# Kernel tuning notes

Measured on AMD Instinct MI355X. Metric: run time of the kernel, lower is better.

## Reference

```python
import jax, jax.numpy as jnp
import numpy as np

N_EMBED = 8192
EMBED_DIM = 256
DECAY = 0.99
EPS = 1e-05


def setup_inputs() -> dict:
    key = jax.random.key(0)
    k1, k2 = jax.random.split(key)
    z = jax.random.normal(k1, (16, 32, 32, EMBED_DIM), dtype=jnp.float32)
    weight = jax.random.normal(k2, (N_EMBED, EMBED_DIM), dtype=jnp.float32)
    cluster_size = jnp.zeros((N_EMBED,), dtype=jnp.float32)
    embed_avg = weight  # register_buffer initialized as a clone of the embedding weight
    return {"z": z, "weight": weight, "cluster_size": cluster_size, "embed_avg": embed_avg}


def reference(z, weight, cluster_size, embed_avg):
    # use_norm=False -> norm is identity; training=True branch; straight_through=True
    zf = z.reshape(-1, EMBED_DIM)  # [N, D]
    # squared euclidean distance: ||z||^2 + ||e||^2 - 2 z.e
    d = (jnp.sum(zf * zf, axis=1, keepdims=True)
         + jnp.sum(weight * weight, axis=1)
         - 2.0 * jnp.einsum('bd,nd->bn', zf, weight))  # [N, K]
    idx = jnp.argmin(d, axis=1)  # [N]
    z_q = weight[idx].reshape(z.shape)
    # commitment loss (z_q detached)
    loss = jnp.mean((jax.lax.stop_gradient(z_q) - z) ** 2)
    # straight-through estimator
    z_q_st = z + jax.lax.stop_gradient(z_q - z)
    # --- EMA codebook update (no_grad in torch) ---
    counts = jax.ops.segment_sum(jnp.ones_like(idx, dtype=jnp.float32), idx, num_segments=N_EMBED)
    dw = jax.ops.segment_sum(zf, idx, num_segments=N_EMBED)  # == onehot.T @ zf
    new_cluster_size = DECAY * cluster_size + (1.0 - DECAY) * counts
    new_embed_avg = DECAY * embed_avg + (1.0 - DECAY) * dw
    n = jnp.sum(new_cluster_size)
    cs = (new_cluster_size + EPS) / (n + N_EMBED * EPS) * n
    new_weight = new_embed_avg / cs[:, None]
    idx_out = idx.reshape(z.shape[:-1])
    return (z_q_st, loss, idx_out,
            jax.lax.stop_gradient(new_weight),
            jax.lax.stop_gradient(new_cluster_size),
            jax.lax.stop_gradient(new_embed_avg))
```

## Files before the change

### kernel.cpp

```cpp
#include <hip/hip_runtime.h>
#include <cstdint>
#include <cstddef>

#define N_PTS   16384
#define K_CODES 8192
#define DIM     256
#define DECAYF  0.99f
#define OMDF    0.01f
#define EPSF    1e-5f

#define OFF_ZQ   0
#define OFF_LOSS 4194304
#define OFF_IDX  4194305
#define OFF_W    4210689
#define OFF_CS   6307841
#define OFF_EA   6316033

#define ZB_OFF   OFF_ZQ
#define WB_OFF   (OFF_ZQ + 2097152)
#define HEN_OFF  (OFF_ZQ + 3145728)
#define C1_OFF   OFF_W
#define C2_OFF   (OFF_W + 1048576)

typedef __attribute__((ext_vector_type(8))) short bf16x8;
typedef __attribute__((ext_vector_type(4))) float f32x4;

__device__ inline unsigned short f2b(float f) {
    unsigned u = __float_as_uint(f);
    return (unsigned short)((u + 0x7FFFu + ((u >> 16) & 1u)) >> 16);
}

__device__ inline unsigned umaxu(unsigned a, unsigned b) { return a > b ? a : b; }
__device__ inline unsigned uminu(unsigned a, unsigned b) { return a < b ? a : b; }

__device__ inline void gload16(const void* g, void* l) {
    __builtin_amdgcn_global_load_lds(
        (const __attribute__((address_space(1))) unsigned int*)g,
        (__attribute__((address_space(3))) unsigned int*)l, 16, 0, 0);
}

__global__ void k_cvt2(const float* __restrict__ z, short* __restrict__ zb,
                       const float* __restrict__ w, short* __restrict__ wb,
                       float* __restrict__ hen, unsigned* __restrict__ cnt,
                       float* __restrict__ zn2) {
    const int tid = threadIdx.x;
    if (blockIdx.x < N_PTS * DIM / 2048) {
        size_t base = (size_t)(blockIdx.x * 256 + tid) * 8;
        float4 a = *(const float4*)(z + base);
        float4 b = *(const float4*)(z + base + 4);
        bf16x8 o;
        o[0] = (short)f2b(128.f * a.x); o[1] = (short)f2b(128.f * a.y);
        o[2] = (short)f2b(128.f * a.z); o[3] = (short)f2b(128.f * a.w);
        o[4] = (short)f2b(128.f * b.x); o[5] = (short)f2b(128.f * b.y);
        o[6] = (short)f2b(128.f * b.z); o[7] = (short)f2b(128.f * b.w);
        *(bf16x8*)(zb + base) = o;
        float s = a.x * a.x + a.y * a.y + a.z * a.z + a.w * a.w
                + b.x * b.x + b.y * b.y + b.z * b.z + b.w * b.w;
        #pragma unroll
        for (int m = 16; m >= 1; m >>= 1) s += __shfl_xor(s, m, 64);
        if ((tid & 31) == 0) zn2[blockIdx.x * 8 + (tid >> 5)] = s;
    } else {
        int blk = blockIdx.x - N_PTS * DIM / 2048;
        size_t base = (size_t)(blk * 256 + tid) * 8;
        float4 a = *(const float4*)(w + base);
        float4 b = *(const float4*)(w + base + 4);
        bf16x8 o;
        o[0] = (short)f2b(a.x); o[1] = (short)f2b(a.y);
        o[2] = (short)f2b(a.z); o[3] = (short)f2b(a.w);
        o[4] = (short)f2b(b.x); o[5] = (short)f2b(b.y);
        o[6] = (short)f2b(b.z); o[7] = (short)f2b(b.w);
        *(bf16x8*)(wb + base) = o;
        float s = a.x * a.x + a.y * a.y + a.z * a.z + a.w * a.w
                + b.x * b.x + b.y * b.y + b.z * b.z + b.w * b.w;
        #pragma unroll
        for (int m = 16; m >= 1; m >>= 1) s += __shfl_xor(s, m, 64);
        if ((tid & 31) == 0) hen[base >> 8] = 0.5f * s;
        int gid = blk * 256 + tid;
        if (gid < K_CODES) cnt[gid] = 0u;
    }
}

__global__ __launch_bounds__(256, 4) void k_gemm(const short* __restrict__ zb,
                                                 const short* __restrict__ wb,
                                                 const float* __restrict__ hen,
                                                 unsigned* __restrict__ c1,
                                                 unsigned* __restrict__ c2) {
    __shared__ __align__(16) short As[128 * 64];
    __shared__ __align__(16) short Bs[128 * 64];

    const int tid  = threadIdx.x;
    const int lane = tid & 63;
    const int wv   = tid >> 6;
    const int ztile = blockIdx.x & 127;
    const int kt    = blockIdx.x >> 7;
    const int z0 = ztile * 128, k0 = kt * 128;
    const int col = lane & 15;

    f32x4 acc[2][8];
    #pragma unroll
    for (int ni = 0; ni < 8; ni++) {
        float h = 131072.0f - 128.0f * hen[k0 + ni * 16 + col];
        f32x4 iv = {h, h, h, h};
        acc[0][ni] = iv; acc[1][ni] = iv;
    }
    const unsigned inv0 = (unsigned)(K_CODES - 1 - (k0 + col));

    const int srow = lane >> 3;
    const int scol = ((lane & 7) ^ srow) * 8;

    #pragma unroll
    for (int dc = 0; dc < 4; ++dc) {
        __syncthreads();
        #pragma unroll
        for (int s4 = 0; s4 < 4; ++s4) {
            int seg = wv * 4 + s4;
            gload16(zb + (size_t)(z0 + seg * 8 + srow) * DIM + dc * 64 + scol,
                    As + seg * 512 + lane * 8);
            gload16(wb + (size_t)(k0 + seg * 8 + srow) * DIM + dc * 64 + scol,
                    Bs + seg * 512 + lane * 8);
        }
        __syncthreads();
        #pragma unroll
        for (int kk = 0; kk < 2; ++kk) {
            int ch = ((kk << 2) + (lane >> 4)) ^ (lane & 7);
            bf16x8 a0 = *(const bf16x8*)&As[(wv * 32 + col) * 64 + ch * 8];
            bf16x8 a1 = *(const bf16x8*)&As[(wv * 32 + 16 + col) * 64 + ch * 8];
            #pragma unroll
            for (int ni = 0; ni < 8; ni++) {
                bf16x8 b = *(const bf16x8*)&Bs[(ni * 16 + col) * 64 + ch * 8];
                acc[0][ni] = __builtin_amdgcn_mfma_f32_16x16x32_bf16(
                    a0, b, acc[0][ni], 0, 0, 0);
                acc[1][ni] = __builtin_amdgcn_mfma_f32_16x16x32_bf16(
                    a1, b, acc[1][ni], 0, 0, 0);
            }
        }
    }

    #pragma unroll
    for (int mi = 0; mi < 2; mi++) {
        #pragma unroll
        for (int r = 0; r < 4; r++) {
            unsigned k8[8];
            #pragma unroll
            for (int ni = 0; ni < 8; ni++) {
                unsigned q = (unsigned)acc[mi][ni][r];
                k8[ni] = (q << 13) | (inv0 - 16u * ni);
            }
            unsigned p1 = umaxu(k8[0], k8[1]), q1 = uminu(k8[0], k8[1]);
            unsigned p2 = umaxu(k8[2], k8[3]), q2 = uminu(k8[2], k8[3]);
            unsigned p3 = umaxu(k8[4], k8[5]), q3 = uminu(k8[4], k8[5]);
            unsigned p4 = umaxu(k8[6], k8[7]), q4 = uminu(k8[6], k8[7]);
            unsigned a1 = umaxu(p1, p2);
            unsigned a2 = umaxu(uminu(p1, p2), umaxu(q1, q2));
            unsigned b1 = umaxu(p3, p4);
            unsigned b2 = umaxu(uminu(p3, p4), umaxu(q3, q4));
            unsigned t1 = umaxu(a1, b1);
            unsigned t2 = umaxu(uminu(a1, b1), umaxu(a2, b2));
            unsigned m1 = t1;
            #pragma unroll
            for (int m = 8; m >= 1; m >>= 1)
                m1 = umaxu(m1, (unsigned)__shfl_xor((int)m1, m, 64));
            unsigned cc = (t1 == m1) ? t2 : t1;
            #pragma unroll
            for (int m = 8; m >= 1; m >>= 1)
                cc = umaxu(cc, (unsigned)__shfl_xor((int)cc, m, 64));
            if (col == 0) {
                int row = wv * 32 + mi * 16 + (lane >> 4) * 4 + r;
                c1[(size_t)kt * N_PTS + z0 + row] = m1;
                c2[(size_t)kt * N_PTS + z0 + row] = cc;
            }
        }
    }
}

__global__ __launch_bounds__(256) void k_rescore(
        const float* __restrict__ z, const float* __restrict__ w,
        const unsigned* __restrict__ c1, const unsigned* __restrict__ c2,
        const float* __restrict__ zn2,
        float* __restrict__ out,
        unsigned* __restrict__ cnt, float* __restrict__ lossp) {
    __shared__ unsigned s1[64 * 5], s2[64 * 5];
    const int t  = threadIdx.x;
    const int w0 = blockIdx.x * 4;
    {
        int kt = t >> 2, wo = t & 3;
        s1[kt * 5 + wo] = c1[(size_t)kt * N_PTS + w0 + wo];
        s2[kt * 5 + wo] = c2[(size_t)kt * N_PTS + w0 + wo];
    }
    __syncthreads();
    const int wv   = t >> 6;
    const int lane = t & 63;
    const int wid  = w0 + wv;
    unsigned k1 = s1[lane * 5 + wv];
    unsigned k2 = s2[lane * 5 + wv];

    unsigned m1 = k1;
    #pragma unroll
    for (int m = 32; m >= 1; m >>= 1)
        m1 = umaxu(m1, (unsigned)__shfl_xor((int)m1, m, 64));
    unsigned e = (k1 == m1) ? k2 : k1;
    unsigned m2 = e;
    #pragma unroll
    for (int m = 32; m >= 1; m >>= 1)
        m2 = umaxu(m2, (unsigned)__shfl_xor((int)m2, m, 64));

    int idx = K_CODES - 1 - (int)(m1 & 0x1FFFu);
    float scf = ((float)(int)(m1 >> 13) - 131072.0f) * 0.0078125f;

    unsigned qthr = (m1 >> 13) - 96u;
    if ((m2 >> 13) >= qthr) {
        unsigned long long best = 0ULL;
        float bsc = 0.f;
        #pragma unroll
        for (int j = 0; j < 2; j++) {
            unsigned cj = j ? k2 : k1;
            unsigned long long mask = __ballot((cj >> 13) >= qthr);
            while (mask) {
                int l = __ffsll((unsigned long long)mask) - 1;
                mask &= mask - 1;
                unsigned cwd = (unsigned)__shfl((int)cj, l, 64);
                int k = K_CODES - 1 - (int)(cwd & 0x1FFFu);
                float4 wr = *(const float4*)(w + (size_t)k * DIM + lane * 4);
                float s = 0.f, h = 0.f;
                {
                    const float* zr = z + (size_t)wid * DIM + lane * 4;
                    float4 zv = *(const float4*)zr;
                    s = zv.x * wr.x + zv.y * wr.y + zv.z * wr.z + zv.w * wr.w;
                    h = wr.x * wr.x + wr.y * wr.y + wr.z * wr.z + wr.w * wr.w;
                }
                #pragma unroll
                for (int m = 32; m >= 1; m >>= 1) {
                    s += __shfl_xor(s, m, 64);
                    h += __shfl_xor(h, m, 64);
                }
                float sc = s - 0.5f * h;
                unsigned u = __float_as_uint(sc);
                u = (u & 0x80000000u) ? ~u : (u | 0x80000000u);
                unsigned long long key = ((unsigned long long)u << 32)
                                       | (unsigned)(K_CODES - 1 - k);
                bool better = key > best;
                best = better ? key : best;
                bsc  = better ? sc  : bsc;
            }
        }
        idx = K_CODES - 1 - (int)(unsigned)(best & 0xFFFFFFFFull);
        scf = bsc;
    }

    if (lane == 0) {
        out[OFF_IDX + wid] = (float)idx;
        lossp[wid] = zn2[wid] - 2.0f * scf;
        atomicAdd(cnt + idx, 1u);
    }
}

__global__ __launch_bounds__(1024) void k_prefix(const float* __restrict__ csin,
                                                 float* __restrict__ out,
                                                 const unsigned* __restrict__ cnt,
                                                 unsigned* __restrict__ offs,
                                                 unsigned* __restrict__ list,
                                                 const float* __restrict__ lossp,
                                                 float* __restrict__ nval) {
    __shared__ unsigned scur[K_CODES];
    __shared__ unsigned wtot[16], wbase[16];
    __shared__ float fred[16], fred2[16];
    int t = threadIdx.x, lane = t & 63, wv = t >> 6;
    int base = t * 8;
    unsigned c[8], mysum = 0;
    #pragma unroll
    for (int i = 0; i < 8; i++) { c[i] = cnt[base + i]; mysum += c[i]; }
    unsigned inc = mysum;
    #pragma unroll
    for (int off = 1; off < 64; off <<= 1) {
        unsigned v = (unsigned)__shfl_up((int)inc, off, 64);
        if (lane >= off) inc += v;
    }
    if (lane == 63) wtot[wv] = inc;
    __syncthreads();
    if (t == 0) {
        unsigned r = 0;
        for (int i = 0; i < 16; i++) { wbase[i] = r; r += wtot[i]; }
        offs[K_CODES] = r;
    }
    __syncthreads();
    unsigned my0 = wbase[wv] + inc - mysum;
    float csl = 0.f;
    #pragma unroll
    for (int i = 0; i < 8; i++) {
        offs[base + i] = my0;
        scur[base + i] = my0;
        my0 += c[i];
        float ncs = DECAYF * csin[base + i] + OMDF * (float)c[i];
        out[OFF_CS + base + i] = ncs;
        csl += ncs;
    }
    #pragma unroll
    for (int m = 32; m >= 1; m >>= 1) csl += __shfl_xor(csl, m, 64);
    if (lane == 0) fred[wv] = csl;
    float lp = 0.f;
    #pragma unroll
    for (int i = 0; i < 16; i++) lp += lossp[t + i * 1024];
    #pragma unroll
    for (int m = 32; m >= 1; m >>= 1) lp += __shfl_xor(lp, m, 64);
    if (lane == 0) fred2[wv] = lp;
    __syncthreads();
    if (t == 0) {
        float n = 0.f, L = 0.f;
        for (int i = 0; i < 16; i++) { n += fred[i]; L += fred2[i]; }
        *nval = n;
        out[OFF_LOSS] = L * (1.0f / ((float)N_PTS * DIM));
    }
    {
        int idxs[16];
        #pragma unroll
        for (int j = 0; j < 16; j++)
            idxs[j] = (int)out[OFF_IDX + t + j * 1024];
        #pragma unroll
        for (int j = 0; j < 16; j++) {
            unsigned pos = atomicAdd(&scur[idxs[j]], 1u);
            list[pos] = (unsigned)(t + j * 1024);
        }
    }
}

__global__ __launch_bounds__(256) void k_gather(
        const float* __restrict__ z, const float* __restrict__ ea,
        const float* __restrict__ w,
        float* __restrict__ out,
        const unsigned* __restrict__ offs,
        const unsigned* __restrict__ list,
        const float* __restrict__ nval) {
    __shared__ float sacc[4][256];
    const int k    = blockIdx.x;
    const int lane = threadIdx.x & 63;
    const int wvi  = threadIdx.x >> 6;
    const unsigned beg = offs[k], end = offs[k + 1];
    float4 wr4 = *(const float4*)(w + (size_t)k * DIM + lane * 4);
    float ax = 0.f, ay = 0.f, az = 0.f, aw = 0.f;
    for (unsigned p = beg + wvi; p < end; p += 4) {
        unsigned i = list[p];
        float4 zv = *(const float4*)(z + (size_t)i * DIM + lane * 4);
        ax += zv.x; ay += zv.y; az += zv.z; aw += zv.w;
        *(float4*)(out + OFF_ZQ + (size_t)i * DIM + lane * 4) = wr4;
    }
    {
        float4 t4 = {ax, ay, az, aw};
        *(float4*)&sacc[wvi][lane * 4] = t4;
    }
    __syncthreads();
    const int d = wvi * 64 + lane;
    float s = ((sacc[0][d] + sacc[1][d]) + sacc[2][d]) + sacc[3][d];
    float e = ea[(size_t)k * DIM + d];
    e = DECAYF * e + OMDF * s;
    out[OFF_EA + (size_t)k * DIM + d] = e;

    float cs = out[OFF_CS + k];
    float n  = *nval;
    float inv = 1.f / ((cs + EPSF) / (n + (float)K_CODES * EPSF) * n);
    out[OFF_W + (size_t)k * DIM + d] = e * inv;
}

extern "C" void kernel_launch(void* const* d_in, const int* in_sizes, int n_in,
                              void* d_out, int out_size, void* d_ws, size_t ws_size,
                              hipStream_t stream) {
    const float* z  = (const float*)d_in[0];
    const float* w  = (const float*)d_in[1];
    const float* cs = (const float*)d_in[2];
    const float* ea = (const float*)d_in[3];
    float* out = (float*)d_out;

    short*    zb  = (short*)(out + ZB_OFF);
    short*    wb  = (short*)(out + WB_OFF);
    float*    hen = out + HEN_OFF;
    unsigned* c1  = (unsigned*)(out + C1_OFF);
    unsigned* c2  = (unsigned*)(out + C2_OFF);

    unsigned* cnt   = (unsigned*)d_ws;
    unsigned* offs  = cnt + 8192;
    unsigned* list  = offs + 8200;
    float*    lossp = (float*)(list + 16384);
    float*    nval  = lossp + 16384;
    float*    zn2   = nval + 1;

    hipLaunchKernelGGL(k_cvt2,    dim3((N_PTS + K_CODES) * DIM / 2048), dim3(256), 0, stream,
                       z, zb, w, wb, hen, cnt, zn2);
    hipLaunchKernelGGL(k_gemm,    dim3((N_PTS / 128) * (K_CODES / 128)), dim3(256), 0, stream,
                       zb, wb, hen, c1, c2);
    hipLaunchKernelGGL(k_rescore, dim3(N_PTS / 4),            dim3(256), 0, stream,
                       z, w, c1, c2, zn2, out, cnt, lossp);
    hipLaunchKernelGGL(k_prefix,  dim3(1),                    dim3(1024), 0, stream,
                       cs, out, cnt, offs, list, lossp, nval);
    hipLaunchKernelGGL(k_gather,  dim3(K_CODES),              dim3(256), 0, stream,
                       z, ea, w, out, offs, list, nval);
}
```

Measured before the change: 239.8 us.

## Record per-point slot via atomic return and write z_q in rescore

The rescore kernel now keeps the return value of the per-code count atomic as each point's slot within its code bucket, stored in scratch space inside the output's embed_avg region. The single-block prefix kernel then places points into the sorted list with plain indexed stores instead of shared-memory atomics. The z_q output write moves from the gather kernel to rescore, so each point is written contiguously by its own wave. The z row load in the rescore loop is also hoisted out of the candidate loop. This shortens the serial single-block stage and simplifies gather, at the cost of an extra scratch array and an extra w row read per point in rescore.

```diff
diff --git a/kernel.cpp b/kernel.cpp
--- a/kernel.cpp
+++ b/kernel.cpp
@@ -178,7 +178,8 @@
         const unsigned* __restrict__ c1, const unsigned* __restrict__ c2,
         const float* __restrict__ zn2,
         float* __restrict__ out,
-        unsigned* __restrict__ cnt, float* __restrict__ lossp) {
+        unsigned* __restrict__ cnt, float* __restrict__ lossp,
+        unsigned* __restrict__ ord) {
     __shared__ unsigned s1[64 * 5], s2[64 * 5];
     const int t  = threadIdx.x;
     const int w0 = blockIdx.x * 4;
@@ -211,6 +212,7 @@
     if ((m2 >> 13) >= qthr) {
         unsigned long long best = 0ULL;
         float bsc = 0.f;
+        const float4 zv = *(const float4*)(z + (size_t)wid * DIM + lane * 4);
         #pragma unroll
         for (int j = 0; j < 2; j++) {
             unsigned cj = j ? k2 : k1;
@@ -221,13 +223,8 @@
                 unsigned cwd = (unsigned)__shfl((int)cj, l, 64);
                 int k = K_CODES - 1 - (int)(cwd & 0x1FFFu);
                 float4 wr = *(const float4*)(w + (size_t)k * DIM + lane * 4);
-                float s = 0.f, h = 0.f;
-                {
-                    const float* zr = z + (size_t)wid * DIM + lane * 4;
-                    float4 zv = *(const float4*)zr;
-                    s = zv.x * wr.x + zv.y * wr.y + zv.z * wr.z + zv.w * wr.w;
-                    h = wr.x * wr.x + wr.y * wr.y + wr.z * wr.z + wr.w * wr.w;
-                }
+                float s = zv.x * wr.x + zv.y * wr.y + zv.z * wr.z + zv.w * wr.w;
+                float h = wr.x * wr.x + wr.y * wr.y + wr.z * wr.z + wr.w * wr.w;
                 #pragma unroll
                 for (int m = 32; m >= 1; m >>= 1) {
                     s += __shfl_xor(s, m, 64);
@@ -250,7 +247,11 @@
     if (lane == 0) {
         out[OFF_IDX + wid] = (float)idx;
         lossp[wid] = zn2[wid] - 2.0f * scf;
-        atomicAdd(cnt + idx, 1u);
+        ord[wid] = atomicAdd(cnt + idx, 1u);
+    }
+    {
+        float4 wr = *(const float4*)(w + (size_t)idx * DIM + lane * 4);
+        *(float4*)(out + OFF_ZQ + (size_t)wid * DIM + lane * 4) = wr;
     }
 }
 
@@ -260,8 +261,9 @@
                                                  unsigned* __restrict__ offs,
                                                  unsigned* __restrict__ list,
                                                  const float* __restrict__ lossp,
-                                                 float* __restrict__ nval) {
-    __shared__ unsigned scur[K_CODES];
+                                                 float* __restrict__ nval,
+                                                 const unsigned* __restrict__ ord) {
+    __shared__ unsigned soff[K_CODES];
     __shared__ unsigned wtot[16], wbase[16];
     __shared__ float fred[16], fred2[16];
     int t = threadIdx.x, lane = t & 63, wv = t >> 6;
@@ -288,7 +290,7 @@
     #pragma unroll
     for (int i = 0; i < 8; i++) {
         offs[base + i] = my0;
-        scur[base + i] = my0;
+        soff[base + i] = my0;
         my0 += c[i];
         float ncs = DECAYF * csin[base + i] + OMDF * (float)c[i];
         out[OFF_CS + base + i] = ncs;
@@ -311,21 +313,20 @@
         out[OFF_LOSS] = L * (1.0f / ((float)N_PTS * DIM));
     }
     {
-        int idxs[16];
+        int idxs[16]; unsigned ords[16];
+        #pragma unroll
+        for (int j = 0; j < 16; j++) {
+            idxs[j] = (int)out[OFF_IDX + t + j * 1024];
+            ords[j] = ord[t + j * 1024];
+        }
         #pragma unroll
         for (int j = 0; j < 16; j++)
-            idxs[j] = (int)out[OFF_IDX + t + j * 1024];
-        #pragma unroll
-        for (int j = 0; j < 16; j++) {
-            unsigned pos = atomicAdd(&scur[idxs[j]], 1u);
-            list[pos] = (unsigned)(t + j * 1024);
-        }
+            list[soff[idxs[j]] + ords[j]] = (unsigned)(t + j * 1024);
     }
 }
 
 __global__ __launch_bounds__(256) void k_gather(
         const float* __restrict__ z, const float* __restrict__ ea,
-        const float* __restrict__ w,
         float* __restrict__ out,
         const unsigned* __restrict__ offs,
         const unsigned* __restrict__ list,
@@ -335,13 +336,11 @@
     const int lane = threadIdx.x & 63;
     const int wvi  = threadIdx.x >> 6;
     const unsigned beg = offs[k], end = offs[k + 1];
-    float4 wr4 = *(const float4*)(w + (size_t)k * DIM + lane * 4);
     float ax = 0.f, ay = 0.f, az = 0.f, aw = 0.f;
     for (unsigned p = beg + wvi; p < end; p += 4) {
         unsigned i = list[p];
         float4 zv = *(const float4*)(z + (size_t)i * DIM + lane * 4);
         ax += zv.x; ay += zv.y; az += zv.z; aw += zv.w;
-        *(float4*)(out + OFF_ZQ + (size_t)i * DIM + lane * 4) = wr4;
     }
     {
         float4 t4 = {ax, ay, az, aw};
@@ -374,6 +373,7 @@
     float*    hen = out + HEN_OFF;
     unsigned* c1  = (unsigned*)(out + C1_OFF);
     unsigned* c2  = (unsigned*)(out + C2_OFF);
+    unsigned* ordp = (unsigned*)(out + OFF_EA);
 
     unsigned* cnt   = (unsigned*)d_ws;
     unsigned* offs  = cnt + 8192;
@@ -387,9 +387,9 @@
     hipLaunchKernelGGL(k_gemm,    dim3((N_PTS / 128) * (K_CODES / 128)), dim3(256), 0, stream,
                        zb, wb, hen, c1, c2);
     hipLaunchKernelGGL(k_rescore, dim3(N_PTS / 4),            dim3(256), 0, stream,
-                       z, w, c1, c2, zn2, out, cnt, lossp);
+                       z, w, c1, c2, zn2, out, cnt, lossp, ordp);
     hipLaunchKernelGGL(k_prefix,  dim3(1),                    dim3(1024), 0, stream,
-                       cs, out, cnt, offs, list, lossp, nval);
+                       cs, out, cnt, offs, list, lossp, nval, ordp);
     hipLaunchKernelGGL(k_gather,  dim3(K_CODES),              dim3(256), 0, stream,
-                       z, ea, w, out, offs, list, nval);
-}
+                       z, ea, out, offs, list, nval);
+}
```

Measured after the change: 240.1 us. No clear change (+0.1%).
